# Kernel tuning notes

Hardware: AMD Instinct MI355X
Metric: run time of the kernel (lower is better)

Reference implementation:

```python
import jax, jax.numpy as jnp
import numpy as np

IN_F = 1024
OUT_F = 1024
GRID_SIZE = 8
GRID_LO, GRID_HI = -2.0, 2.0


def _grid_and_inv_denom():
    grid = jnp.linspace(GRID_LO, GRID_HI, GRID_SIZE)  # [G]
    inv_denom = 1.0 / (float((GRID_HI - GRID_LO) / (GRID_SIZE - 1)) + 1e-06)
    return grid, inv_denom


def setup_inputs() -> dict:
    key = jax.random.key(0)
    kx, kw, ks = jax.random.split(key, 3)
    x = jax.random.normal(kx, (4, 2048, IN_F), dtype=jnp.float32)
    # kaiming_uniform_(a=sqrt(5)) on [out,in]: bound = sqrt(6/((1+a^2)*fan_in)) = sqrt(1/fan_in)
    bound = float(np.sqrt(1.0 / IN_F))
    base_w = jax.random.uniform(kw, (OUT_F, IN_F), minval=-bound, maxval=bound, dtype=jnp.float32)
    base_b = jnp.zeros((OUT_F,), dtype=jnp.float32)
    spline_w = 0.02 * jax.random.normal(ks, (OUT_F, IN_F, GRID_SIZE), dtype=jnp.float32)
    return {"x": x, "base_w": base_w, "base_b": base_b, "spline_w": spline_w}


def reference(x, base_w, base_b, spline_w):
    grid, inv_denom = _grid_and_inv_denom()
    lead = x.shape[:-1]
    x_flat = x.reshape(-1, IN_F)  # [B, in]
    # base path: Linear(SiLU(x))
    base_out = jax.nn.silu(x_flat) @ base_w.T + base_b  # [B, out]
    # RBF basis expansion: [B, in, G]
    basis = jnp.exp(-(((x_flat[..., None] - grid) * inv_denom) ** 2))
    spline_out = jnp.einsum('big,oig->bo', basis, spline_w)  # [B, out]
    out = base_out + spline_out
    return out.reshape(*lead, OUT_F)
```

## Files before the change

### kernel.cpp

```cpp
#include <hip/hip_runtime.h>
#include <stdint.h>

namespace {

constexpr int IN_F = 1024;
constexpr int OUT_F = 1024;
constexpr int GSZ = 8;
constexpr int KTOT = IN_F + IN_F * GSZ;
constexpr int BK = 64;
constexpr int NT = KTOT / BK;
constexpr int NBASE = IN_F / BK;

constexpr int BM = 128, BN = 256;
constexpr int NBLK = OUT_F / BN;
constexpr size_t IMG_BYTES = (size_t)BN * BK * 2;
constexpr size_t WS_NEEDED = (size_t)NBLK * NT * IMG_BYTES;

constexpr double H_D     = 4.0 / 7.0;
constexpr double INVD_D  = 1.0 / (H_D + 1e-6);
constexpr double L2E_D   = 1.4426950408889634;
constexpr double SQL2E_D = 1.2011224087864498;
constexpr double CS_D    = INVD_D * SQL2E_D;
constexpr double DLT_D   = H_D * CS_D;

using short8 = __attribute__((ext_vector_type(8))) short;
using f32x4  = __attribute__((ext_vector_type(4))) float;

__device__ __forceinline__ unsigned cvt_pk(float lo, float hi) {
  unsigned r;
  asm("v_cvt_pk_bf16_f32 %0, %1, %2" : "=v"(r) : "v"(lo), "v"(hi));
  return r;
}
__device__ __forceinline__ float silu_f(float v) {
  float e = __builtin_amdgcn_exp2f(-v * (float)L2E_D);
  return v * __builtin_amdgcn_rcpf(1.0f + e);
}
__device__ __forceinline__ int swz(int row, int kk) {
  return (row * 128 + kk * 2) ^ ((row & 7) << 4);
}

__global__ void wprep(const float* __restrict__ bw, const float* __restrict__ sw,
                      char* __restrict__ wimg)
{
  const int total = NBLK * NT * BN * 8;
  for (int idx = blockIdx.x * blockDim.x + threadIdx.x; idx < total;
       idx += gridDim.x * blockDim.x) {
    const int kk8  = idx & 7;
    const int row  = (idx >> 3) & (BN - 1);
    const int rest = idx >> 11;
    const int step = rest % NT;
    const int nb   = rest / NT;
    const int o    = nb * BN + row;
    const int k    = step * BK + kk8 * 8;
    const float* src = (k < IN_F)
      ? (bw + (size_t)o * IN_F + k)
      : (sw + (size_t)o * (size_t)(IN_F * GSZ) + (k - IN_F));
    const float4 a = ((const float4*)src)[0];
    const float4 b = ((const float4*)src)[1];
    int4 v;
    v.x = (int)cvt_pk(a.x, a.y);
    v.y = (int)cvt_pk(a.z, a.w);
    v.z = (int)cvt_pk(b.x, b.y);
    v.w = (int)cvt_pk(b.z, b.w);
    *(int4*)(wimg + (size_t)rest * IMG_BYTES + swz(row, kk8 * 8)) = v;
  }
}

__global__ __launch_bounds__(512)
void kan_fast(const float* __restrict__ x, const float* __restrict__ bb,
              const char* __restrict__ wimg, float* __restrict__ out)
{
  __shared__ char tA[BM * BK * 2];
  __shared__ char tB[2][BN * BK * 2];

  const int t    = threadIdx.x;
  const int lane = t & 63;
  const int wid  = t >> 6;
  const int wr   = (wid >> 2) * 64;
  const int wc   = (wid & 3) * 64;
  const int bm0  = blockIdx.y * BM;
  const char* img = wimg + (size_t)blockIdx.x * NT * IMG_BYTES;
  const int bn0  = blockIdx.x * BN;

  const float CSf  = (float)CS_D;
  const float C0f  = (float)(-2.0 * CS_D);
  const float TDLT = (float)(2.0 * DLT_D);
  float Kc[7];
#pragma unroll
  for (int g = 0; g < 7; ++g) {
    const double cg  = (-2.0 + g * H_D) * CS_D;
    const double cg1 = (-2.0 + (g + 1) * H_D) * CS_D;
    Kc[g] = __builtin_amdgcn_exp2f((float)(-DLT_D * (cg + cg1)));
  }

  f32x4 acc[4][4];
#pragma unroll
  for (int m = 0; m < 4; ++m)
#pragma unroll
    for (int n = 0; n < 4; ++n) acc[m][n] = (f32x4)0.0f;

  float4 rX[4];

  auto issue_B = [&](int step, int buf) {
    const char* g = img + (size_t)step * IMG_BYTES + t * 16;
    char* l = tB[buf] + t * 16;
#pragma unroll
    for (int j = 0; j < 4; ++j)
      __builtin_amdgcn_global_load_lds(
        (const __attribute__((address_space(1))) void*)(g + j * 8192),
        (__attribute__((address_space(3))) void*)(l + j * 8192), 16, 0, 0);
  };

  auto load_x = [&](int step) {
    const int k0  = step * BK;
    const int row = t >> 2;
    if (k0 < IN_F) {
      const float* p = x + (size_t)(bm0 + row) * IN_F + k0 + (t & 3) * 16;
#pragma unroll
      for (int j = 0; j < 4; ++j) rX[j] = ((const float4*)p)[j];
    } else {
      const int i0 = (k0 - IN_F) >> 3;
      const float2 v = *(const float2*)(x + (size_t)(bm0 + row) * IN_F + i0 + (t & 3) * 2);
      rX[0].x = v.x; rX[0].y = v.y;
    }
  };

  auto store_A = [&](int step) {
    const int row = t >> 2;
    if (step < NBASE) {
      unsigned q[8];
#pragma unroll
      for (int j = 0; j < 4; ++j) {
        q[2 * j]     = cvt_pk(silu_f(rX[j].x), silu_f(rX[j].y));
        q[2 * j + 1] = cvt_pk(silu_f(rX[j].z), silu_f(rX[j].w));
      }
      const int kc0 = (t & 3) * 16;
      *(int4*)(tA + swz(row, kc0))     = make_int4(q[0], q[1], q[2], q[3]);
      *(int4*)(tA + swz(row, kc0 + 8)) = make_int4(q[4], q[5], q[6], q[7]);
    } else {
#pragma unroll
      for (int c = 0; c < 2; ++c) {
        const float xv = c ? rX[0].y : rX[0].x;
        const float tb = xv * CSf;
        const float d0 = tb - C0f;
        float e = __builtin_amdgcn_exp2f(-(d0 * d0));
        const float r = __builtin_amdgcn_exp2f(tb * TDLT);
        unsigned q[4];
#pragma unroll
        for (int g = 0; g < 4; ++g) {
          const float a = e;
          const float b = a * r * Kc[2 * g];
          q[g] = cvt_pk(a, b);
          if (g < 3) e = b * r * Kc[2 * g + 1];
        }
        const int iloc = (t & 3) * 2 + c;
        *(int4*)(tA + swz(row, iloc * 8)) = make_int4(q[0], q[1], q[2], q[3]);
      }
    }
  };

  auto compute = [&](int buf) {
    const int r  = lane & 15;
    const int kq = (lane >> 4) * 8;
#pragma unroll
    for (int kh = 0; kh < 2; ++kh) {
      short8 af[4], bf[4];
#pragma unroll
      for (int m = 0; m < 4; ++m)
        af[m] = *(const short8*)(tA + swz(wr + m * 16 + r, kh * 32 + kq));
#pragma unroll
      for (int n = 0; n < 4; ++n)
        bf[n] = *(const short8*)(tB[buf] + swz(wc + n * 16 + r, kh * 32 + kq));
#pragma unroll
      for (int m = 0; m < 4; ++m)
#pragma unroll
        for (int n = 0; n < 4; ++n)
          acc[m][n] = __builtin_amdgcn_mfma_f32_16x16x32_bf16(af[m], bf[n], acc[m][n], 0, 0, 0);
    }
  };

  issue_B(0, 0);
  load_x(0);
  int cur = 0;
  for (int step = 0; step < NT; ++step) {
    store_A(step);
    __syncthreads();
    if (step + 1 < NT) {
      issue_B(step + 1, cur ^ 1);
      load_x(step + 1);
    }
    compute(cur);
    __syncthreads();
    cur ^= 1;
  }

  const int col = lane & 15;
  const int rr  = (lane >> 4) * 4;
#pragma unroll
  for (int m = 0; m < 4; ++m) {
    const int gr = bm0 + wr + m * 16 + rr;
#pragma unroll
    for (int n = 0; n < 4; ++n) {
      const int gc = bn0 + wc + n * 16 + col;
      const float bias = bb[gc];
#pragma unroll
      for (int j = 0; j < 4; ++j)
        out[(size_t)(gr + j) * OUT_F + gc] = acc[m][n][j] + bias;
    }
  }
}

constexpr int SLDK = 64 + 8;

__device__ __forceinline__ unsigned f2bf(float f) {
  unsigned u = __float_as_uint(f);
  return (u + 0x7fffu + ((u >> 16) & 1u)) >> 16;
}
__device__ __forceinline__ unsigned pk2(float lo, float hi) {
  return f2bf(lo) | (f2bf(hi) << 16);
}

__global__ __launch_bounds__(256)
void kan_slow(const float* __restrict__ x, const float* __restrict__ bw,
              const float* __restrict__ bb, const float* __restrict__ sw,
              float* __restrict__ out)
{
  __shared__ unsigned short tA[128][SLDK];
  __shared__ unsigned short tB[128][SLDK];

  const int t    = threadIdx.x;
  const int lane = t & 63;
  const int wid  = t >> 6;
  const int wr   = (wid >> 1) * 64;
  const int wc   = (wid & 1) * 64;
  const int bm0  = blockIdx.x * 128;
  const int bn0  = blockIdx.y * 128;

  const float CS = (float)CS_D;
  float gsc[GSZ];
#pragma unroll
  for (int g = 0; g < GSZ; ++g)
    gsc[g] = (float)((-2.0 + g * H_D) * CS_D);

  f32x4 acc[4][4];
#pragma unroll
  for (int m = 0; m < 4; ++m)
#pragma unroll
    for (int n = 0; n < 4; ++n) acc[m][n] = (f32x4)0.0f;

  float4 rA[8], rB[8];
  const int rw = t >> 4;
  const int cw = (t & 15) * 4;

  auto load_tile = [&](int step) {
    const int k0 = step * BK;
    const bool base = (k0 < IN_F);
#pragma unroll
    for (int j = 0; j < 8; ++j) {
      const int row = j * 16 + rw;
      const float* p = base
        ? (bw + (size_t)(bn0 + row) * IN_F + k0 + cw)
        : (sw + (size_t)(bn0 + row) * (size_t)(IN_F * GSZ) + (k0 - IN_F) + cw);
      rB[j] = *(const float4*)p;
    }
    if (base) {
#pragma unroll
      for (int j = 0; j < 8; ++j) {
        const int row = j * 16 + rw;
        rA[j] = *(const float4*)(x + (size_t)(bm0 + row) * IN_F + k0 + cw);
      }
    } else {
      const int i0  = (k0 - IN_F) >> 3;
      const int row = t >> 1;
      rA[0] = *(const float4*)(x + (size_t)(bm0 + row) * IN_F + i0 + (t & 1) * 4);
    }
  };

  auto store_tile = [&](int step) {
    const int k0 = step * BK;
    const bool base = (k0 < IN_F);
#pragma unroll
    for (int j = 0; j < 8; ++j) {
      const int row = j * 16 + rw;
      uint2 v;
      v.x = pk2(rB[j].x, rB[j].y);
      v.y = pk2(rB[j].z, rB[j].w);
      *(uint2*)&tB[row][cw] = v;
    }
    if (base) {
#pragma unroll
      for (int j = 0; j < 8; ++j) {
        const int row = j * 16 + rw;
        uint2 v;
        v.x = pk2(silu_f(rA[j].x), silu_f(rA[j].y));
        v.y = pk2(silu_f(rA[j].z), silu_f(rA[j].w));
        *(uint2*)&tA[row][cw] = v;
      }
    } else {
      const int row  = t >> 1;
      const int half = t & 1;
      const float* xv = (const float*)&rA[0];
#pragma unroll
      for (int c = 0; c < 4; ++c) {
        const float tb = xv[c] * CS;
        union { unsigned u[4]; int4 v4; } pkv;
#pragma unroll
        for (int g = 0; g < 8; g += 2) {
          const float t0 = tb - gsc[g];
          const float t1 = tb - gsc[g + 1];
          const float e0 = __builtin_amdgcn_exp2f(-(t0 * t0));
          const float e1 = __builtin_amdgcn_exp2f(-(t1 * t1));
          pkv.u[g >> 1] = pk2(e0, e1);
        }
        const int kc = (half * 4 + c) * 8;
        *(int4*)&tA[row][kc] = pkv.v4;
      }
    }
  };

  auto compute_tile = [&]() {
    const int r  = lane & 15;
    const int kq = (lane >> 4) * 8;
#pragma unroll
    for (int kh = 0; kh < 2; ++kh) {
      short8 af[4], bf[4];
#pragma unroll
      for (int m = 0; m < 4; ++m)
        af[m] = *(const short8*)&tA[wr + m * 16 + r][kh * 32 + kq];
#pragma unroll
      for (int n = 0; n < 4; ++n)
        bf[n] = *(const short8*)&tB[wc + n * 16 + r][kh * 32 + kq];
#pragma unroll
      for (int m = 0; m < 4; ++m)
#pragma unroll
        for (int n = 0; n < 4; ++n)
          acc[m][n] = __builtin_amdgcn_mfma_f32_16x16x32_bf16(af[m], bf[n], acc[m][n], 0, 0, 0);
    }
  };

  load_tile(0);
  for (int step = 0; step < NT; ++step) {
    store_tile(step);
    __syncthreads();
    if (step + 1 < NT) load_tile(step + 1);
    compute_tile();
    __syncthreads();
  }

  const int col = lane & 15;
  const int rr  = (lane >> 4) * 4;
#pragma unroll
  for (int m = 0; m < 4; ++m) {
    const int gr = bm0 + wr + m * 16 + rr;
#pragma unroll
    for (int n = 0; n < 4; ++n) {
      const int gc = bn0 + wc + n * 16 + col;
      const float bias = bb[gc];
#pragma unroll
      for (int j = 0; j < 4; ++j)
        out[(size_t)(gr + j) * OUT_F + gc] = acc[m][n][j] + bias;
    }
  }
}

}

extern "C" void kernel_launch(void* const* d_in, const int* in_sizes, int n_in,
                              void* d_out, int out_size, void* d_ws, size_t ws_size,
                              hipStream_t stream) {
  const float *x, *bw, *bb, *sw;
  if (in_sizes[0] == OUT_F) {
    bb = (const float*)d_in[0];
    bw = (const float*)d_in[1];
    sw = (const float*)d_in[2];
    x  = (const float*)d_in[3];
  } else {
    x  = (const float*)d_in[0];
    bw = (const float*)d_in[1];
    bb = (const float*)d_in[2];
    sw = (const float*)d_in[3];
  }
  float* out = (float*)d_out;
  const int rows = (in_sizes[0] == OUT_F) ? in_sizes[3] / IN_F : in_sizes[0] / IN_F;

  if (ws_size >= WS_NEEDED && d_ws != nullptr && (rows % BM) == 0) {
    hipLaunchKernelGGL(wprep, dim3(2048), dim3(256), 0, stream, bw, sw, (char*)d_ws);
    dim3 grid(NBLK, rows / BM);
    hipLaunchKernelGGL(kan_fast, grid, dim3(512), 0, stream,
                       x, bb, (const char*)d_ws, out);
  } else {
    dim3 grid(rows / 128, OUT_F / 128);
    hipLaunchKernelGGL(kan_slow, grid, dim3(256), 0, stream, x, bw, bb, sw, out);
  }
}
```

Baseline: 227.5 us.

## Double-buffer A tile and interleave loads with split MFMA phases

Double-buffers the A tile in LDS and prefetches x two steps ahead in alternating register sets. Each K-step is split into two MFMA half-phases, with B loads and A conversion for the next step placed between them. It also adds s_setprio around the MFMA bursts and requests two blocks per CU through launch_bounds. The aim is to hide global-load and exp/convert latency behind matrix work, at the cost of extra LDS use and register pressure from the 2-occupancy cap.

```diff
diff --git a/kernel.cpp b/kernel.cpp
--- a/kernel.cpp
+++ b/kernel.cpp
@@ -66,11 +66,11 @@
   }
 }
 
-__global__ __launch_bounds__(512)
+__global__ __launch_bounds__(512, 2)
 void kan_fast(const float* __restrict__ x, const float* __restrict__ bb,
               const char* __restrict__ wimg, float* __restrict__ out)
 {
-  __shared__ char tA[BM * BK * 2];
+  __shared__ char tA[2][BM * BK * 2];
   __shared__ char tB[2][BN * BK * 2];
 
   const int t    = threadIdx.x;
@@ -99,48 +99,48 @@
 #pragma unroll
     for (int n = 0; n < 4; ++n) acc[m][n] = (f32x4)0.0f;
 
-  float4 rX[4];
-
-  auto issue_B = [&](int step, int buf) {
-    const char* g = img + (size_t)step * IMG_BYTES + t * 16;
-    char* l = tB[buf] + t * 16;
-#pragma unroll
-    for (int j = 0; j < 4; ++j)
+  float4 xE[4], xO[4];
+
+  auto issue_B2 = [&](int step, char* dstB, int half) {
+    const char* g = img + (size_t)step * IMG_BYTES + half * 16384 + t * 16;
+    char* l = dstB + half * 16384 + t * 16;
+#pragma unroll
+    for (int j = 0; j < 2; ++j)
       __builtin_amdgcn_global_load_lds(
         (const __attribute__((address_space(1))) void*)(g + j * 8192),
         (__attribute__((address_space(3))) void*)(l + j * 8192), 16, 0, 0);
   };
 
-  auto load_x = [&](int step) {
+  auto load_x = [&](int step, float4 (&xr)[4]) {
     const int k0  = step * BK;
     const int row = t >> 2;
     if (k0 < IN_F) {
       const float* p = x + (size_t)(bm0 + row) * IN_F + k0 + (t & 3) * 16;
 #pragma unroll
-      for (int j = 0; j < 4; ++j) rX[j] = ((const float4*)p)[j];
+      for (int j = 0; j < 4; ++j) xr[j] = ((const float4*)p)[j];
     } else {
       const int i0 = (k0 - IN_F) >> 3;
       const float2 v = *(const float2*)(x + (size_t)(bm0 + row) * IN_F + i0 + (t & 3) * 2);
-      rX[0].x = v.x; rX[0].y = v.y;
-    }
-  };
-
-  auto store_A = [&](int step) {
+      xr[0].x = v.x; xr[0].y = v.y;
+    }
+  };
+
+  auto conv_A = [&](int step, const float4 (&xr)[4], char* dstA) {
     const int row = t >> 2;
     if (step < NBASE) {
       unsigned q[8];
 #pragma unroll
       for (int j = 0; j < 4; ++j) {
-        q[2 * j]     = cvt_pk(silu_f(rX[j].x), silu_f(rX[j].y));
-        q[2 * j + 1] = cvt_pk(silu_f(rX[j].z), silu_f(rX[j].w));
+        q[2 * j]     = cvt_pk(silu_f(xr[j].x), silu_f(xr[j].y));
+        q[2 * j + 1] = cvt_pk(silu_f(xr[j].z), silu_f(xr[j].w));
       }
       const int kc0 = (t & 3) * 16;
-      *(int4*)(tA + swz(row, kc0))     = make_int4(q[0], q[1], q[2], q[3]);
-      *(int4*)(tA + swz(row, kc0 + 8)) = make_int4(q[4], q[5], q[6], q[7]);
+      *(int4*)(dstA + swz(row, kc0))     = make_int4(q[0], q[1], q[2], q[3]);
+      *(int4*)(dstA + swz(row, kc0 + 8)) = make_int4(q[4], q[5], q[6], q[7]);
     } else {
 #pragma unroll
       for (int c = 0; c < 2; ++c) {
-        const float xv = c ? rX[0].y : rX[0].x;
+        const float xv = c ? xr[0].y : xr[0].x;
         const float tb = xv * CSf;
         const float d0 = tb - C0f;
         float e = __builtin_amdgcn_exp2f(-(d0 * d0));
@@ -154,44 +154,73 @@
           if (g < 3) e = b * r * Kc[2 * g + 1];
         }
         const int iloc = (t & 3) * 2 + c;
-        *(int4*)(tA + swz(row, iloc * 8)) = make_int4(q[0], q[1], q[2], q[3]);
+        *(int4*)(dstA + swz(row, iloc * 8)) = make_int4(q[0], q[1], q[2], q[3]);
       }
     }
   };
 
-  auto compute = [&](int buf) {
+  auto read_frags = [&](const char* A, const char* B, int kh,
+                        short8 (&af)[4], short8 (&bf)[4]) {
     const int r  = lane & 15;
     const int kq = (lane >> 4) * 8;
 #pragma unroll
-    for (int kh = 0; kh < 2; ++kh) {
+    for (int m = 0; m < 4; ++m)
+      af[m] = *(const short8*)(A + swz(wr + m * 16 + r, kh * 32 + kq));
+#pragma unroll
+    for (int n = 0; n < 4; ++n)
+      bf[n] = *(const short8*)(B + swz(wc + n * 16 + r, kh * 32 + kq));
+  };
+
+  auto mfma16 = [&](short8 (&af)[4], short8 (&bf)[4]) {
+#pragma unroll
+    for (int m = 0; m < 4; ++m)
+#pragma unroll
+      for (int n = 0; n < 4; ++n)
+        acc[m][n] = __builtin_amdgcn_mfma_f32_16x16x32_bf16(af[m], bf[n], acc[m][n], 0, 0, 0);
+  };
+
+  auto step_body = [&](int s, char* curA, char* curB, char* nxtA, char* nxtB,
+                       const float4 (&xconv)[4], float4 (&xload)[4]) {
+    if (s + 1 < NT) issue_B2(s + 1, nxtB, 0);
+    if (s + 2 < NT) load_x(s + 2, xload);
+    {
       short8 af[4], bf[4];
-#pragma unroll
-      for (int m = 0; m < 4; ++m)
-        af[m] = *(const short8*)(tA + swz(wr + m * 16 + r, kh * 32 + kq));
-#pragma unroll
-      for (int n = 0; n < 4; ++n)
-        bf[n] = *(const short8*)(tB[buf] + swz(wc + n * 16 + r, kh * 32 + kq));
-#pragma unroll
-      for (int m = 0; m < 4; ++m)
-#pragma unroll
-        for (int n = 0; n < 4; ++n)
-          acc[m][n] = __builtin_amdgcn_mfma_f32_16x16x32_bf16(af[m], bf[n], acc[m][n], 0, 0, 0);
-    }
-  };
-
-  issue_B(0, 0);
-  load_x(0);
-  int cur = 0;
-  for (int step = 0; step < NT; ++step) {
-    store_A(step);
+      read_frags(curA, curB, 0, af, bf);
+      __builtin_amdgcn_s_barrier();
+      asm volatile("s_waitcnt lgkmcnt(0)" ::: "memory");
+      __builtin_amdgcn_sched_barrier(0);
+      __builtin_amdgcn_s_setprio(1);
+      mfma16(af, bf);
+      __builtin_amdgcn_s_setprio(0);
+      __builtin_amdgcn_s_barrier();
+    }
+    if (s + 1 < NT) {
+      issue_B2(s + 1, nxtB, 1);
+      conv_A(s + 1, xconv, nxtA);
+    }
+    {
+      short8 af[4], bf[4];
+      read_frags(curA, curB, 1, af, bf);
+      __builtin_amdgcn_s_barrier();
+      asm volatile("s_waitcnt lgkmcnt(0)" ::: "memory");
+      __builtin_amdgcn_sched_barrier(0);
+      __builtin_amdgcn_s_setprio(1);
+      mfma16(af, bf);
+      __builtin_amdgcn_s_setprio(0);
+    }
     __syncthreads();
-    if (step + 1 < NT) {
-      issue_B(step + 1, cur ^ 1);
-      load_x(step + 1);
-    }
-    compute(cur);
-    __syncthreads();
-    cur ^= 1;
+  };
+
+  load_x(0, xE);
+  load_x(1, xO);
+  issue_B2(0, tB[0], 0);
+  issue_B2(0, tB[0], 1);
+  conv_A(0, xE, tA[0]);
+  __syncthreads();
+
+  for (int s = 0; s < NT; s += 2) {
+    step_body(s,     tA[0], tB[0], tA[1], tB[1], xO, xE);
+    step_body(s + 1, tA[1], tB[1], tA[0], tB[0], xE, xO);
   }
 
   const int col = lane & 15;
```

Measured after the change: 187.7 us. -17.5%, faster.

## Warp-specialize GEMM into producer and consumer waves with double-buffered A

Applied to the files above, without the earlier changes.

The kernel now splits its waves into roles. Four waves only issue the weight loads into LDS and build the SiLU/RBF bf16 A tile for the next step. The other four waves only run MFMAs on the current buffers. The A tile is double-buffered and the M tile is halved to 64, with a launch-bounds hint for higher occupancy, so basis generation and loads overlap with matrix math. In exchange, half the waves do no MFMA work, the manual waitcnt counts must stay correct, and the grid has twice as many blocks, each reading the same weight image.

```diff
diff --git a/kernel.cpp b/kernel.cpp
--- a/kernel.cpp
+++ b/kernel.cpp
@@ -11,7 +11,7 @@
 constexpr int NT = KTOT / BK;
 constexpr int NBASE = IN_F / BK;
 
-constexpr int BM = 128, BN = 256;
+constexpr int BM = 64, BN = 256;
 constexpr int NBLK = OUT_F / BN;
 constexpr size_t IMG_BYTES = (size_t)BN * BK * 2;
 constexpr size_t WS_NEEDED = (size_t)NBLK * NT * IMG_BYTES;
@@ -66,17 +66,17 @@
   }
 }
 
-__global__ __launch_bounds__(512)
+__global__ __launch_bounds__(512, 4)
 void kan_fast(const float* __restrict__ x, const float* __restrict__ bb,
               const char* __restrict__ wimg, float* __restrict__ out)
 {
-  __shared__ char tA[BM * BK * 2];
+  __shared__ char tA[2][BM * BK * 2];
   __shared__ char tB[2][BN * BK * 2];
 
   const int t    = threadIdx.x;
   const int lane = t & 63;
   const int wid  = t >> 6;
-  const int wr   = (wid >> 2) * 64;
+  const bool cons = (wid < 4);
   const int wc   = (wid & 3) * 64;
   const int bm0  = blockIdx.y * BM;
   const char* img = wimg + (size_t)blockIdx.x * NT * IMG_BYTES;
@@ -99,48 +99,51 @@
 #pragma unroll
     for (int n = 0; n < 4; ++n) acc[m][n] = (f32x4)0.0f;
 
-  float4 rX[4];
-
-  auto issue_B = [&](int step, int buf) {
-    const char* g = img + (size_t)step * IMG_BYTES + t * 16;
-    char* l = tB[buf] + t * 16;
-#pragma unroll
-    for (int j = 0; j < 4; ++j)
+  const int t2   = t & 255;
+  const int prow = t2 >> 2;
+  const int pcol = t2 & 3;
+  const int pw   = wid & 3;
+
+  float4 xr[4];
+
+  auto issue_B = [&](int step, char* dstB) {
+    const char* g = img + (size_t)step * IMG_BYTES + pw * 8192 + lane * 16;
+    char* l = dstB + pw * 8192 + lane * 16;
+#pragma unroll
+    for (int j = 0; j < 8; ++j)
       __builtin_amdgcn_global_load_lds(
-        (const __attribute__((address_space(1))) void*)(g + j * 8192),
-        (__attribute__((address_space(3))) void*)(l + j * 8192), 16, 0, 0);
+        (const __attribute__((address_space(1))) void*)(g + j * 1024),
+        (__attribute__((address_space(3))) void*)(l + j * 1024), 16, 0, 0);
   };
 
   auto load_x = [&](int step) {
-    const int k0  = step * BK;
-    const int row = t >> 2;
+    const int k0 = step * BK;
     if (k0 < IN_F) {
-      const float* p = x + (size_t)(bm0 + row) * IN_F + k0 + (t & 3) * 16;
-#pragma unroll
-      for (int j = 0; j < 4; ++j) rX[j] = ((const float4*)p)[j];
+      const float* p = x + (size_t)(bm0 + prow) * IN_F + k0 + pcol * 16;
+#pragma unroll
+      for (int j = 0; j < 4; ++j) xr[j] = ((const float4*)p)[j];
     } else {
       const int i0 = (k0 - IN_F) >> 3;
-      const float2 v = *(const float2*)(x + (size_t)(bm0 + row) * IN_F + i0 + (t & 3) * 2);
-      rX[0].x = v.x; rX[0].y = v.y;
-    }
-  };
-
-  auto store_A = [&](int step) {
-    const int row = t >> 2;
+      const float2 v = *(const float2*)(x + (size_t)(bm0 + prow) * IN_F + i0 + pcol * 2);
+      xr[0].x = v.x; xr[0].y = v.y;
+    }
+  };
+
+  auto conv_A = [&](int step, char* dstA) {
     if (step < NBASE) {
       unsigned q[8];
 #pragma unroll
       for (int j = 0; j < 4; ++j) {
-        q[2 * j]     = cvt_pk(silu_f(rX[j].x), silu_f(rX[j].y));
-        q[2 * j + 1] = cvt_pk(silu_f(rX[j].z), silu_f(rX[j].w));
-      }
-      const int kc0 = (t & 3) * 16;
-      *(int4*)(tA + swz(row, kc0))     = make_int4(q[0], q[1], q[2], q[3]);
-      *(int4*)(tA + swz(row, kc0 + 8)) = make_int4(q[4], q[5], q[6], q[7]);
+        q[2 * j]     = cvt_pk(silu_f(xr[j].x), silu_f(xr[j].y));
+        q[2 * j + 1] = cvt_pk(silu_f(xr[j].z), silu_f(xr[j].w));
+      }
+      const int kc0 = pcol * 16;
+      *(int4*)(dstA + swz(prow, kc0))     = make_int4(q[0], q[1], q[2], q[3]);
+      *(int4*)(dstA + swz(prow, kc0 + 8)) = make_int4(q[4], q[5], q[6], q[7]);
     } else {
 #pragma unroll
       for (int c = 0; c < 2; ++c) {
-        const float xv = c ? rX[0].y : rX[0].x;
+        const float xv = c ? xr[0].y : xr[0].x;
         const float tb = xv * CSf;
         const float d0 = tb - C0f;
         float e = __builtin_amdgcn_exp2f(-(d0 * d0));
@@ -153,59 +156,89 @@
           q[g] = cvt_pk(a, b);
           if (g < 3) e = b * r * Kc[2 * g + 1];
         }
-        const int iloc = (t & 3) * 2 + c;
-        *(int4*)(tA + swz(row, iloc * 8)) = make_int4(q[0], q[1], q[2], q[3]);
-      }
-    }
-  };
-
-  auto compute = [&](int buf) {
-    const int r  = lane & 15;
-    const int kq = (lane >> 4) * 8;
+        *(int4*)(dstA + swz(prow, (pcol * 2 + c) * 8)) = make_int4(q[0], q[1], q[2], q[3]);
+      }
+    }
+  };
+
+  auto prod_drain = [&](int s) {
+    if (s + 2 < NBASE) {
+      asm volatile("s_waitcnt vmcnt(4) lgkmcnt(0)" ::: "memory");
+    } else if (s + 2 < NT) {
+      asm volatile("s_waitcnt vmcnt(1) lgkmcnt(0)" ::: "memory");
+    } else {
+      asm volatile("s_waitcnt vmcnt(0) lgkmcnt(0)" ::: "memory");
+    }
+    __builtin_amdgcn_sched_barrier(0);
+  };
+
+  const int fr = lane & 15;
+  const int kq = (lane >> 4) * 8;
+
+  auto consume = [&](const char* curA, const char* curB) {
+    short8 af[4], bf[4];
+    __builtin_amdgcn_s_setprio(1);
 #pragma unroll
     for (int kh = 0; kh < 2; ++kh) {
-      short8 af[4], bf[4];
 #pragma unroll
       for (int m = 0; m < 4; ++m)
-        af[m] = *(const short8*)(tA + swz(wr + m * 16 + r, kh * 32 + kq));
+        af[m] = *(const short8*)(curA + swz(m * 16 + fr, kh * 32 + kq));
 #pragma unroll
       for (int n = 0; n < 4; ++n)
-        bf[n] = *(const short8*)(tB[buf] + swz(wc + n * 16 + r, kh * 32 + kq));
+        bf[n] = *(const short8*)(curB + swz(wc + n * 16 + fr, kh * 32 + kq));
 #pragma unroll
       for (int m = 0; m < 4; ++m)
 #pragma unroll
         for (int n = 0; n < 4; ++n)
           acc[m][n] = __builtin_amdgcn_mfma_f32_16x16x32_bf16(af[m], bf[n], acc[m][n], 0, 0, 0);
     }
-  };
-
-  issue_B(0, 0);
-  load_x(0);
+    __builtin_amdgcn_s_setprio(0);
+  };
+
+  if (!cons) {
+    load_x(0);
+    conv_A(0, tA[0]);
+    issue_B(0, tB[0]);
+    load_x(1);
+    asm volatile("s_waitcnt vmcnt(0) lgkmcnt(0)" ::: "memory");
+    __builtin_amdgcn_sched_barrier(0);
+  }
+  __builtin_amdgcn_s_barrier();
+
   int cur = 0;
-  for (int step = 0; step < NT; ++step) {
-    store_A(step);
-    __syncthreads();
-    if (step + 1 < NT) {
-      issue_B(step + 1, cur ^ 1);
-      load_x(step + 1);
-    }
-    compute(cur);
-    __syncthreads();
+  for (int s = 0; s < NT; ++s) {
+    char* curA = tA[cur];
+    char* curB = tB[cur];
+    char* nxtA = tA[cur ^ 1];
+    char* nxtB = tB[cur ^ 1];
+    if (cons) {
+      consume(curA, curB);
+    } else {
+      if (s + 1 < NT) {
+        issue_B(s + 1, nxtB);
+        conv_A(s + 1, nxtA);
+        if (s + 2 < NT) load_x(s + 2);
+        prod_drain(s);
+      }
+    }
+    __builtin_amdgcn_s_barrier();
     cur ^= 1;
   }
 
-  const int col = lane & 15;
-  const int rr  = (lane >> 4) * 4;
-#pragma unroll
-  for (int m = 0; m < 4; ++m) {
-    const int gr = bm0 + wr + m * 16 + rr;
-#pragma unroll
-    for (int n = 0; n < 4; ++n) {
-      const int gc = bn0 + wc + n * 16 + col;
-      const float bias = bb[gc];
-#pragma unroll
-      for (int j = 0; j < 4; ++j)
-        out[(size_t)(gr + j) * OUT_F + gc] = acc[m][n][j] + bias;
+  if (cons) {
+    const int col = lane & 15;
+    const int rr  = (lane >> 4) * 4;
+#pragma unroll
+    for (int m = 0; m < 4; ++m) {
+      const int gr = bm0 + m * 16 + rr;
+#pragma unroll
+      for (int n = 0; n < 4; ++n) {
+        const int gc = bn0 + wc + n * 16 + col;
+        const float bias = bb[gc];
+#pragma unroll
+        for (int j = 0; j < 4; ++j)
+          out[(size_t)(gr + j) * OUT_F + gc] = acc[m][n][j] + bias;
+      }
     }
   }
 }
```

Result: faster. 198.5 us (-12.8%).
